# Kernel optimization log

Measured on AMD Instinct MI355X. Metric: run time of the kernel, lower is better.

The kernel has to match this reference:

```python
import jax, jax.numpy as jnp
import numpy as np

V = 25; NE = 5; DIM = 192; H = 6; HD = 32; N = 64; T = 64
SCALE = HD ** -0.5
COEFF = 0.4
NTU_EDGES = [(1,2),(2,21),(3,21),(4,3),(5,21),(6,5),(7,6),(8,7),(9,21),(10,9),(11,10),(12,11),(13,1),(14,13),(15,14),(16,15),(17,1),(18,17),(19,18),(20,19),(22,23),(23,8),(24,25),(25,12)]

def _compute_hops():
    # replicate MHSA.__init__ hop-distance computation (A = [I, adj, adj] summed+binarized)
    adj = np.zeros((V, V))
    for i, j in NTU_EDGES:
        adj[i-1, j-1] = 1.0; adj[j-1, i-1] = 1.0
    h1 = ((np.eye(V) + adj) != 0).astype(np.float64)
    h = [None] * V
    h[0] = np.eye(V); h[1] = h1
    hops = np.zeros((V, V))
    for i in range(2, V):
        h[i] = ((h[i-1] @ h1.T) != 0).astype(np.float64)
    for i in range(V-1, 0, -1):
        if np.any(h[i] - h[i-1]):
            h[i] = h[i] - h[i-1]
            hops += i * h[i]
    return hops.astype(np.int32)

def setup_inputs() -> dict:
    key = jax.random.key(0)
    ks = jax.random.split(key, 12)
    hops = jnp.asarray(_compute_hops())
    n_hop = int(hops.max()) + 1
    std = 0.02
    return {
        "x": jax.random.normal(ks[0], (N, DIM, T, V), jnp.float32),
        "joint_label": jnp.arange(V, dtype=jnp.int32) % NE,  # all 5 hyperedge labels present
        "groups": NE,  # unused by forward (kept for signature fidelity)
        "he_weight": jax.random.uniform(ks[1], (NE,), jnp.float32),
        "hops": hops,
        "ln_g": jnp.ones((DIM,), jnp.float32),
        "ln_b": jnp.zeros((DIM,), jnp.float32),
        "hgc_w": std * jax.random.normal(ks[2], (DIM, DIM), jnp.float32),
        "q_w": std * jax.random.normal(ks[3], (DIM, DIM), jnp.float32),
        "kv_w": std * jax.random.normal(ks[4], (2 * DIM, DIM), jnp.float32),
        "proj_w": std * jax.random.normal(ks[5], (DIM, HD), jnp.float32),  # grouped 1x1 conv, groups=6
        "proj_b": jnp.zeros((DIM,), jnp.float32),
        "rpe": std * jax.random.normal(ks[6], (n_hop, DIM), jnp.float32),
        "w1": std * jax.random.normal(ks[7], (H, HD), jnp.float32),
        "outer": jnp.tile(jnp.eye(V, dtype=jnp.float32), (H, 1, 1)) + std * jax.random.normal(ks[8], (H, V, V), jnp.float32),
        "alpha": 0.1 * jnp.ones((1,), jnp.float32),
        "lin1_w": std * jax.random.normal(ks[9], (T // 5, T), jnp.float32),
        "lin1_b": jnp.zeros((T // 5,), jnp.float32),
        "lin2_w": std * jax.random.normal(ks[10], (T, T // 5), jnp.float32),
        "lin2_b": jnp.zeros((T,), jnp.float32),
    }

def _forward(x, joint_label, he_weight, hops, ln_g, ln_b, hgc_w, q_w, kv_w, proj_w, proj_b, rpe, w1, outer, alpha, lin1_w, lin1_b, lin2_w, lin2_b):
    N_, C, T_, V_ = x.shape
    # ---- HGattn branch: hypergraph conv + temporal squeeze-excite gate ----
    label = jax.nn.one_hot(joint_label, NE, dtype=x.dtype)            # (V, 5)
    label1 = label / label.sum(0, keepdims=True)
    label1 = label1 / jnp.sqrt(label.sum(1, keepdims=True))
    label1 = (he_weight[None, :] * label1).T                          # (5, V)
    norm_label = label / label.sum(1, keepdims=True)
    h_adj = norm_label @ label1                                       # (V, V)
    z = jnp.einsum('nctv,vw->nctw', x, h_adj)
    op = jnp.einsum('nctv,oc->notv', z, hgc_w)                        # (N, dim, T, V) 1x1 conv
    op_tr = op.transpose(0, 1, 3, 2)                                  # (N, dim, V, T)
    s = op_tr.mean(axis=(1, 2))                                       # (N, T) global avg pool over (dim, V)
    g = jax.nn.sigmoid(jax.nn.relu(s @ lin1_w.T + lin1_b) @ lin2_w.T + lin2_b)  # (N, T)
    op_final = op_tr + COEFF * (op_tr * g[:, None, None, :])
    e = op_final.transpose(0, 1, 3, 2)                                # (N, dim, T, V)
    # ---- LayerNorm over channel dim ----
    xc = x.transpose(0, 2, 3, 1)                                      # (N, T, V, C)
    mu = xc.mean(-1, keepdims=True)
    var = xc.var(-1, keepdims=True)
    xn = (((xc - mu) / jnp.sqrt(var + 1e-5)) * ln_g + ln_b).transpose(0, 3, 1, 2)
    # ---- MHSA with hop-indexed relative bias, e-branch scores, outer fusion ----
    q = jnp.einsum('nctv,oc->notv', xn, q_w).reshape(N_, H, HD, T_, V_).transpose(0, 3, 1, 4, 2)   # (N,T,H,V,hd)
    kv = jnp.einsum('nctv,oc->notv', xn, kv_w).reshape(N_, 2, H, HD, T_, V_)
    k = kv[:, 0].transpose(0, 3, 1, 4, 2)
    v = kv[:, 1].transpose(0, 3, 1, 4, 2)
    e_k = e.reshape(N_, H, HD, T_, V_).transpose(0, 3, 1, 4, 2)
    k_r = rpe[hops].reshape(V_, V_, H, HD)                            # hop-distance relative position table
    b = jnp.einsum('bthnc,nmhc->bthnm', q, k_r)
    c = jnp.einsum('bthnc,bthmc->bthnm', q, e_k)
    d = jnp.einsum('hc,bthmc->bthm', w1, e_k)[..., None, :]
    a = jnp.einsum('bthnc,bthmc->bthnm', q, k)
    attn = jax.nn.softmax((a + b + c + d) * SCALE, axis=-1)
    o = jnp.einsum('bthnm,bthmc->bthnc', alpha * attn + outer[None, None], v)
    o = o.transpose(0, 1, 2, 4, 3).reshape(N_, T_, DIM, V_).transpose(0, 2, 1, 3)  # (N, dim, T, V)
    # grouped 1x1 conv projection (groups = H)
    og = o.reshape(N_, H, HD, T_, V_)
    wg = proj_w.reshape(H, HD, HD)
    o = jnp.einsum('ngitv,goi->ngotv', og, wg).reshape(N_, DIM, T_, V_) + proj_b[None, :, None, None]
    return x + o  # dim_in == dim -> identity skip

def reference(x, joint_label, groups, he_weight, hops, ln_g, ln_b, hgc_w, q_w, kv_w, proj_w, proj_b, rpe, w1, outer, alpha, lin1_w, lin1_b, lin2_w, lin2_b):
    return _forward(x, joint_label, he_weight, hops, ln_g, ln_b, hgc_w, q_w, kv_w, proj_w, proj_b, rpe, w1, outer, alpha, lin1_w, lin1_b, lin2_w, lin2_b)
```

## Files before the change

kernel.cpp:

```cpp
#include <hip/hip_runtime.h>
#include <hip/hip_bf16.h>

using bf16 = __hip_bfloat16;
typedef __bf16 bf16x8 __attribute__((ext_vector_type(8)));
typedef float f32x4 __attribute__((ext_vector_type(4)));

constexpr int kDim = 192;
constexpr int kH = 6;
constexpr int kHd = 32;
constexpr int kN = 64;
constexpr int kT = 64;
constexpr int kV = 25;
constexpr int kP = kT * kV;
constexpr int kNCstride = kDim * kP;
constexpr float kScale = 0.17677669529663687f;
constexpr float kCoeff = 0.4f;

__global__ void __launch_bounds__(256) setup_kernel(
    const int* __restrict__ jl, const float* __restrict__ hew,
    const float* __restrict__ hgc, const float* __restrict__ qw,
    const float* __restrict__ kvw, const float* __restrict__ rpe,
    const float* __restrict__ proj_w, const float* __restrict__ lng,
    const float* __restrict__ lnb, int n_hop, float* __restrict__ hadj,
    bf16* __restrict__ Wb, float* __restrict__ G, float* __restrict__ Bb,
    bf16* __restrict__ RPEb, bf16* __restrict__ pwb, bf16* __restrict__ VT) {
  const int bid = blockIdx.x;
  const int tid = threadIdx.x;
  if (bid < 576) {
    int i = bid * 256 + tid;
    float v;
    if (i < 36864) {
      v = hgc[i];
    } else {
      int local = i - 36864;
      int c = local % kDim;
      v = (local < 36864) ? qw[local] : kvw[local - 36864];
      v *= lng[c];
    }
    Wb[i] = __float2bfloat16(v);
  } else if (bid == 576) {
    __shared__ int lbl[kV];
    __shared__ int cnt[8];
    if (tid < 8) cnt[tid] = 0;
    __syncthreads();
    if (tid < kV) { lbl[tid] = jl[tid]; atomicAdd(&cnt[lbl[tid]], 1); }
    __syncthreads();
    for (int idx = tid; idx < kV * kV; idx += 256) {
      int v = idx / kV, w = idx - v * kV;
      float val = 0.f;
      if (lbl[v] == lbl[w]) val = hew[lbl[v]] / (float)cnt[lbl[v]];
      hadj[idx] = val;
    }
  } else if (bid == 577) {
    for (int i = tid; i < kH * 16 * kHd; i += 256) {
      int h = i >> 9, hp = (i >> 5) & 15, d = i & 31;
      float v = (hp < n_hop) ? rpe[hp * kDim + h * kHd + d] : 0.f;
      RPEb[i] = __float2bfloat16(v);
    }
    for (int i = tid; i < kDim * kHd; i += 256)
      pwb[i] = __float2bfloat16(proj_w[i]);
  } else if (bid < 722) {
    int o = (bid - 578) * 4 + (tid >> 6);
    int lane = tid & 63;
    const float* Wr =
        (o < kDim) ? (qw + (size_t)o * kDim) : (kvw + (size_t)(o - kDim) * kDim);
    float gs = 0.f, bs = 0.f;
    for (int c = lane; c < kDim; c += 64) {
      float wv = Wr[c];
      gs += wv * lng[c];
      bs += wv * lnb[c];
    }
    for (int off = 32; off > 0; off >>= 1) {
      gs += __shfl_down(gs, off);
      bs += __shfl_down(bs, off);
    }
    if (lane == 0) { G[o] = gs; Bb[o] = bs; }
  } else {
    int row = (bid - 722) * 256 + tid;
    if (row < kN * kT * kDim) {
      uint4 z = {0u, 0u, 0u, 0u};
      *reinterpret_cast<uint4*>(reinterpret_cast<char*>(VT) + (size_t)row * 64 +
                                48) = z;
    }
  }
}

__global__ void __launch_bounds__(256) prep_kernel(
    const float* __restrict__ x, bf16* __restrict__ XR, float* __restrict__ mu,
    float* __restrict__ rstd) {
  __shared__ float ps[kV][25], ps2[kV][25];
  const int tid = threadIdx.x;
  const int t = blockIdx.x, n = blockIdx.y;
  const float* xb = x + (size_t)n * kNCstride + t * kV;
  size_t ob = ((size_t)n * kP + t * kV) * kDim;
  for (int idx = tid; idx < 600; idx += 256) {
    int p = idx % 25, c8 = idx / 25;
    float a = 0.f, b = 0.f;
    union { uint4 u; __bf16 h[8]; } pk;
#pragma unroll
    for (int i = 0; i < 8; ++i) {
      float v = xb[(size_t)(c8 * 8 + i) * kP + p];
      a += v;
      b += v * v;
      pk.h[i] = (__bf16)v;
    }
    *reinterpret_cast<uint4*>(XR + ob + (size_t)p * kDim + c8 * 8) = pk.u;
    ps[p][c8] = a;
    ps2[p][c8] = b;
  }
  __syncthreads();
  if (tid < kV) {
    float a = 0.f, b = 0.f;
#pragma unroll
    for (int c8 = 0; c8 < 24; ++c8) { a += ps[tid][c8]; b += ps2[tid][c8]; }
    float m = a * (1.f / kDim);
    float var = b * (1.f / kDim) - m * m;
    int gid = n * kP + t * kV + tid;
    mu[gid] = m;
    rstd[gid] = rsqrtf(var + 1e-5f);
  }
}

template <int OBN, int MOUT, bool VS, bool LNF>
__global__ void __launch_bounds__(64) mfma_gemm_kernel(
    const bf16* __restrict__ A, const bf16* __restrict__ B,
    bf16* __restrict__ out, bf16* __restrict__ VT,
    const float* __restrict__ muA, const float* __restrict__ rsA,
    const float* __restrict__ G, const float* __restrict__ Bb) {
  int id = blockIdx.x;
  int per = gridDim.x >> 3;
  int wg = (id & 7) * per + (id >> 3);
  int n = wg / (25 * OBN);
  int rem = wg - n * (25 * OBN);
  const int pb = (rem / OBN) * 64;
  const int ob = (rem % OBN) * 64;
  const int l = threadIdx.x;
  B += (size_t)n * kNCstride;
  out += (size_t)n * kP * MOUT;
  f32x4 acc[4][4] = {};
  const int lm = l & 15;
  const int lk = (l >> 4) * 8;
  for (int kb = 0; kb < kDim; kb += 32) {
    bf16x8 af[4], bfv[4];
#pragma unroll
    for (int mf = 0; mf < 4; ++mf)
      af[mf] = *reinterpret_cast<const bf16x8*>(
          A + (size_t)(ob + mf * 16 + lm) * kDim + kb + lk);
#pragma unroll
    for (int nf = 0; nf < 4; ++nf)
      bfv[nf] = *reinterpret_cast<const bf16x8*>(
          B + (size_t)(pb + nf * 16 + lm) * kDim + kb + lk);
#pragma unroll
    for (int mf = 0; mf < 4; ++mf)
#pragma unroll
      for (int nf = 0; nf < 4; ++nf)
        acc[mf][nf] = __builtin_amdgcn_mfma_f32_16x16x32_bf16(
            af[mf], bfv[nf], acc[mf][nf], 0, 0, 0);
  }
  const int r0 = (l >> 4) * 4;
  float rsv[4], muv[4];
  if (LNF) {
#pragma unroll
    for (int nf = 0; nf < 4; ++nf) {
      int p = pb + nf * 16 + lm;
      rsv[nf] = rsA[n * kP + p];
      muv[nf] = muA[n * kP + p];
    }
  }
  int tt[4], vv[4];
#pragma unroll
  for (int nf = 0; nf < 4; ++nf) {
    int p = pb + nf * 16 + lm;
    tt[nf] = p / 25;
    vv[nf] = p - tt[nf] * 25;
  }
#pragma unroll
  for (int mf = 0; mf < 4; ++mf) {
    const int o0 = ob + mf * 16 + r0;
    float ga[4] = {0.f, 0.f, 0.f, 0.f}, ba[4] = {0.f, 0.f, 0.f, 0.f};
    if (LNF) {
      float4 g4 = *reinterpret_cast<const float4*>(G + o0);
      float4 b4 = *reinterpret_cast<const float4*>(Bb + o0);
      ga[0] = g4.x; ga[1] = g4.y; ga[2] = g4.z; ga[3] = g4.w;
      ba[0] = b4.x; ba[1] = b4.y; ba[2] = b4.z; ba[3] = b4.w;
    }
    if (!VS || o0 < 384) {
#pragma unroll
      for (int nf = 0; nf < 4; ++nf) {
        const int p = pb + nf * 16 + lm;
        union { uint2 u; bf16 b[4]; } pk;
#pragma unroll
        for (int r = 0; r < 4; ++r) {
          float vvv = acc[mf][nf][r];
          if (LNF) vvv = rsv[nf] * (vvv - muv[nf] * ga[r]) + ba[r];
          pk.b[r] = __float2bfloat16(vvv);
        }
        *reinterpret_cast<uint2*>(out + (size_t)p * MOUT + o0) = pk.u;
      }
    } else {
#pragma unroll
      for (int nf = 0; nf < 4; ++nf) {
        size_t rowb =
            ((size_t)(n * kT + tt[nf]) * kDim + (o0 - 384)) * 32 + vv[nf];
#pragma unroll
        for (int r = 0; r < 4; ++r) {
          float vvv = acc[mf][nf][r];
          if (LNF) vvv = rsv[nf] * (vvv - muv[nf] * ga[r]) + ba[r];
          VT[rowb + (size_t)r * 32] = __float2bfloat16(vvv);
        }
      }
    }
  }
}

__global__ void __launch_bounds__(256) haapply_kernel(
    bf16* __restrict__ OP, const float* __restrict__ hadjg,
    float* __restrict__ s_out) {
  __shared__ ushort tile[kV * kDim];
  __shared__ float ha[640];
  __shared__ float red[4];
  const int tid = threadIdx.x;
  const int t = blockIdx.x, n = blockIdx.y;
  size_t base = ((size_t)n * kP + t * kV) * kDim;
  for (int i = tid; i < kV * kV; i += 256) ha[i] = hadjg[i];
  const uint2* src = reinterpret_cast<const uint2*>(OP + base);
  uint2* dst2 = reinterpret_cast<uint2*>(tile);
  for (int i = tid; i < kV * kDim / 4; i += 256) dst2[i] = src[i];
  __syncthreads();
  float ssum = 0.f;
  for (int idx = tid; idx < 600; idx += 256) {
    int c8 = idx % 24, w = idx / 24;
    float acc[8] = {0.f, 0.f, 0.f, 0.f, 0.f, 0.f, 0.f, 0.f};
    for (int v = 0; v < kV; ++v) {
      float coef = ha[v * kV + w];
      union { uint4 u; __bf16 h[8]; } ld;
      ld.u = *reinterpret_cast<const uint4*>(tile + v * kDim + c8 * 8);
#pragma unroll
      for (int j = 0; j < 8; ++j) acc[j] += coef * (float)ld.h[j];
    }
    union { uint4 u; __bf16 h[8]; } pk;
    float s8 = 0.f;
#pragma unroll
    for (int j = 0; j < 8; ++j) { pk.h[j] = (__bf16)acc[j]; s8 += acc[j]; }
    *reinterpret_cast<uint4*>(OP + base + (size_t)w * kDim + c8 * 8) = pk.u;
    ssum += s8;
  }
  for (int off = 32; off > 0; off >>= 1) ssum += __shfl_down(ssum, off);
  if ((tid & 63) == 0) red[tid >> 6] = ssum;
  __syncthreads();
  if (tid == 0)
    s_out[n * kT + t] = (red[0] + red[1] + red[2] + red[3]) *
                        (1.f / (float)(kDim * kV));
}

__global__ void gate_kernel(const float* __restrict__ s,
                            const float* __restrict__ w1l,
                            const float* __restrict__ b1,
                            const float* __restrict__ w2l,
                            const float* __restrict__ b2,
                            float* __restrict__ gatef) {
  __shared__ float sh[kT];
  __shared__ float hid[12];
  int n = blockIdx.x, t = threadIdx.x;
  sh[t] = s[n * kT + t];
  __syncthreads();
  if (t < 12) {
    float a = b1[t];
    for (int j = 0; j < kT; ++j) a += sh[j] * w1l[t * kT + j];
    hid[t] = fmaxf(a, 0.f);
  }
  __syncthreads();
  float a = b2[t];
  for (int j = 0; j < 12; ++j) a += hid[j] * w2l[t * 12 + j];
  float g = 1.f / (1.f + __expf(-a));
  gatef[n * kT + t] = 1.f + kCoeff * g;
}

__global__ void __launch_bounds__(384) attn_kernel(
    const bf16* __restrict__ QK, const bf16* __restrict__ VT,
    const bf16* __restrict__ OP, const float* __restrict__ gatef,
    const int* __restrict__ hops, const bf16* __restrict__ RPEb,
    const float* __restrict__ w1, const float* __restrict__ outer,
    const float* __restrict__ alpha_p, const bf16* __restrict__ pwb,
    const float* __restrict__ proj_b, const float* __restrict__ x,
    float* __restrict__ out) {
  __shared__ ushort wls[kH][2560];
  __shared__ int hopsS[kV][32];
  const int tid = threadIdx.x;
  const int lane = tid & 63;
  const int h = tid >> 6;
  const int t = blockIdx.x, n = blockIdx.y;
  const int nt = n * kT + t;
  const int lm = lane & 15, g = lane >> 4;

  for (int i = tid; i < kV * 32; i += 384) {
    int v = i >> 5, w = i & 31;
    hopsS[v][w] = (w < kV) ? hops[v * kV + w] : 0;
  }
  __syncthreads();

  bf16* Pp = (bf16*)&wls[h][0];
  bf16* OLp = (bf16*)&wls[h][1280];
  float* QRp = (float*)&wls[h][1280];

  const float f = gatef[nt];
  const float alpha = alpha_p[0];
  const bf16* Qbase = QK + (size_t)(n * kP + t * kV) * 384;
  const bf16* Ebase = OP + (size_t)(n * kP + t * kV) * kDim;
  const int colO = h * kHd + g * 8;

  bf16x8 qf[2], kf[2], ef[2];
#pragma unroll
  for (int mf = 0; mf < 2; ++mf) {
    const bf16* row = Qbase + (size_t)(mf * 16 + lm) * 384;
    qf[mf] = *reinterpret_cast<const bf16x8*>(row + colO);
    kf[mf] = *reinterpret_cast<const bf16x8*>(row + kDim + colO);
    ef[mf] = *reinterpret_cast<const bf16x8*>(
        Ebase + (size_t)(mf * 16 + lm) * kDim + colO);
  }
  bf16x8 rf = *reinterpret_cast<const bf16x8*>(RPEb + (h * 16 + lm) * kHd + g * 8);

  float w1v[8];
  {
    float4 wa = *reinterpret_cast<const float4*>(w1 + h * kHd + g * 8);
    float4 wb = *reinterpret_cast<const float4*>(w1 + h * kHd + g * 8 + 4);
    w1v[0] = wa.x; w1v[1] = wa.y; w1v[2] = wa.z; w1v[3] = wa.w;
    w1v[4] = wb.x; w1v[5] = wb.y; w1v[6] = wb.z; w1v[7] = wb.w;
  }
  float dt[2];
#pragma unroll
  for (int nf = 0; nf < 2; ++nf) {
    float a = 0.f;
#pragma unroll
    for (int j = 0; j < 8; ++j) a += w1v[j] * (float)ef[nf][j];
    a += __shfl_xor(a, 16);
    a += __shfl_xor(a, 32);
    dt[nf] = f * a;
  }

  bf16x8 kef[2];
#pragma unroll
  for (int nf = 0; nf < 2; ++nf)
#pragma unroll
    for (int j = 0; j < 8; ++j)
      kef[nf][j] = (__bf16)((float)kf[nf][j] + f * (float)ef[nf][j]);

  f32x4 aK[2][2] = {};
  f32x4 aR[2] = {};
#pragma unroll
  for (int mf = 0; mf < 2; ++mf) {
#pragma unroll
    for (int nf = 0; nf < 2; ++nf)
      aK[mf][nf] =
          __builtin_amdgcn_mfma_f32_16x16x32_bf16(qf[mf], kef[nf], aK[mf][nf], 0, 0, 0);
    aR[mf] = __builtin_amdgcn_mfma_f32_16x16x32_bf16(qf[mf], rf, aR[mf], 0, 0, 0);
  }

#pragma unroll
  for (int mf = 0; mf < 2; ++mf)
#pragma unroll
    for (int r = 0; r < 4; ++r)
      QRp[(mf * 16 + g * 4 + r) * 18 + lm] = aR[mf][r];

  const bool w1ok = (lm + 16) < kV;
#pragma unroll
  for (int mf = 0; mf < 2; ++mf) {
#pragma unroll
    for (int r = 0; r < 4; ++r) {
      int v = mf * 16 + g * 4 + r;
      int vc = v < kV ? v : kV - 1;
      int hp0 = hopsS[vc][lm];
      int hp1 = hopsS[vc][lm + 16];
      float s0 = (aK[mf][0][r] + QRp[v * 18 + hp0] + dt[0]) * kScale;
      float s1 = (aK[mf][1][r] + QRp[v * 18 + hp1] + dt[1]) * kScale;
      if (!w1ok) s1 = -3.0e38f;
      float m = fmaxf(s0, s1);
#pragma unroll
      for (int d = 1; d < 16; d <<= 1) m = fmaxf(m, __shfl_xor(m, d));
      float e0 = __expf(s0 - m);
      float e1 = w1ok ? __expf(s1 - m) : 0.f;
      float sum = e0 + e1;
#pragma unroll
      for (int d = 1; d < 16; d <<= 1) sum += __shfl_xor(sum, d);
      float inv = alpha / sum;
      float o0 = outer[h * (kV * kV) + vc * kV + lm];
      float o1 = w1ok ? outer[h * (kV * kV) + vc * kV + lm + 16] : 0.f;
      Pp[v * 40 + lm] = __float2bfloat16(e0 * inv + o0);
      Pp[v * 40 + lm + 16] = __float2bfloat16(w1ok ? e1 * inv + o1 : 0.f);
    }
  }

  bf16x8 pa[2], vb[2];
#pragma unroll
  for (int mf = 0; mf < 2; ++mf)
    pa[mf] = *reinterpret_cast<const bf16x8*>(Pp + (mf * 16 + lm) * 40 + g * 8);
#pragma unroll
  for (int nf = 0; nf < 2; ++nf)
    vb[nf] = *reinterpret_cast<const bf16x8*>(
        VT + ((size_t)(nt * kDim + h * kHd + nf * 16 + lm)) * 32 + g * 8);
  f32x4 aO[2][2] = {};
#pragma unroll
  for (int mf = 0; mf < 2; ++mf)
#pragma unroll
    for (int nf = 0; nf < 2; ++nf)
      aO[mf][nf] =
          __builtin_amdgcn_mfma_f32_16x16x32_bf16(pa[mf], vb[nf], aO[mf][nf], 0, 0, 0);

#pragma unroll
  for (int mf = 0; mf < 2; ++mf)
#pragma unroll
    for (int nf = 0; nf < 2; ++nf)
#pragma unroll
      for (int r = 0; r < 4; ++r)
        OLp[(mf * 16 + g * 4 + r) * 40 + nf * 16 + lm] =
            __float2bfloat16(aO[mf][nf][r]);

  bf16x8 oa[2], pwf[2];
#pragma unroll
  for (int nf = 0; nf < 2; ++nf)
    oa[nf] = *reinterpret_cast<const bf16x8*>(OLp + (nf * 16 + lm) * 40 + g * 8);
#pragma unroll
  for (int mf = 0; mf < 2; ++mf)
    pwf[mf] = *reinterpret_cast<const bf16x8*>(pwb +
        (h * kHd + mf * 16 + lm) * kHd + g * 8);
  f32x4 aF[2][2] = {};
#pragma unroll
  for (int mf = 0; mf < 2; ++mf)
#pragma unroll
    for (int nf = 0; nf < 2; ++nf)
      aF[mf][nf] =
          __builtin_amdgcn_mfma_f32_16x16x32_bf16(pwf[mf], oa[nf], aF[mf][nf], 0, 0, 0);

#pragma unroll
  for (int mf = 0; mf < 2; ++mf) {
#pragma unroll
    for (int r = 0; r < 4; ++r) {
      int oo = mf * 16 + g * 4 + r;
      int c = h * kHd + oo;
      float pbv = proj_b[c];
      size_t gbase = (size_t)n * kNCstride + (size_t)c * kP + t * kV;
#pragma unroll
      for (int nf = 0; nf < 2; ++nf) {
        int v = nf * 16 + lm;
        if (v < kV) out[gbase + v] = x[gbase + v] + aF[mf][nf][r] + pbv;
      }
    }
  }
}

extern "C" void kernel_launch(void* const* d_in, const int* in_sizes, int n_in,
                              void* d_out, int out_size, void* d_ws,
                              size_t ws_size, hipStream_t stream) {
  const float* x = (const float*)d_in[0];
  const int* joint_label = (const int*)d_in[1];
  const float* he_weight = (const float*)d_in[3];
  const int* hops = (const int*)d_in[4];
  const float* ln_g = (const float*)d_in[5];
  const float* ln_b = (const float*)d_in[6];
  const float* hgc_w = (const float*)d_in[7];
  const float* q_w = (const float*)d_in[8];
  const float* kv_w = (const float*)d_in[9];
  const float* proj_w = (const float*)d_in[10];
  const float* proj_b = (const float*)d_in[11];
  const float* rpe = (const float*)d_in[12];
  const float* w1 = (const float*)d_in[13];
  const float* outer = (const float*)d_in[14];
  const float* alpha = (const float*)d_in[15];
  const float* lin1_w = (const float*)d_in[16];
  const float* lin1_b = (const float*)d_in[17];
  const float* lin2_w = (const float*)d_in[18];
  const float* lin2_b = (const float*)d_in[19];
  const int n_hop = in_sizes[12] / kDim;

  char* w = (char*)d_ws;
  bf16* QK = (bf16*)w;
  w += (size_t)kN * kP * 2 * kDim * 2;
  bf16* XR = (bf16*)w;
  w += (size_t)kN * kP * kDim * 2;
  bf16* OP = (bf16*)w;
  w += (size_t)kN * kP * kDim * 2;
  w += 65536;
  bf16* VT = (bf16*)w;
  w += (size_t)kN * kT * kDim * 32 * 2;
  bf16* Wb = (bf16*)w;
  w += (size_t)768 * kDim * 2;
  bf16* RPEb = (bf16*)w;
  w += (size_t)kH * 16 * kHd * 2;
  bf16* pwb = (bf16*)w;
  w += (size_t)kDim * kHd * 2;
  float* hadj = (float*)w;
  w += 1024 * 4;
  float* s_ws = (float*)w;
  w += kN * kT * 4;
  float* gatef = (float*)w;
  w += kN * kT * 4;
  float* mu = (float*)w;
  w += (size_t)kN * kP * 4;
  float* rstd = (float*)w;
  w += (size_t)kN * kP * 4;
  float* G = (float*)w;
  w += 576 * 4;
  float* Bb = (float*)w;
  w += 576 * 4;

  hipLaunchKernelGGL(setup_kernel, dim3(3794), dim3(256), 0, stream,
                     joint_label, he_weight, hgc_w, q_w, kv_w, rpe, proj_w,
                     ln_g, ln_b, n_hop, hadj, Wb, G, Bb, RPEb, pwb, VT);
  hipLaunchKernelGGL(prep_kernel, dim3(kT, kN), dim3(256), 0, stream, x, XR,
                     mu, rstd);
  hipLaunchKernelGGL((mfma_gemm_kernel<3, kDim, false, false>),
                     dim3(25 * 3 * kN), dim3(64), 0, stream, Wb, XR, OP,
                     (bf16*)nullptr, nullptr, nullptr, nullptr, nullptr);
  hipLaunchKernelGGL(haapply_kernel, dim3(kT, kN), dim3(256), 0, stream, OP,
                     hadj, s_ws);
  hipLaunchKernelGGL(gate_kernel, dim3(kN), dim3(kT), 0, stream, s_ws, lin1_w,
                     lin1_b, lin2_w, lin2_b, gatef);
  hipLaunchKernelGGL((mfma_gemm_kernel<9, 384, true, true>),
                     dim3(25 * 9 * kN), dim3(64), 0, stream, Wb + 192 * kDim,
                     XR, QK, VT, mu, rstd, G, Bb);
  hipLaunchKernelGGL(attn_kernel, dim3(kT, kN), dim3(384), 0, stream, QK, VT,
                     OP, gatef, hops, RPEb, w1, outer, alpha, pwb, proj_b, x,
                     (float*)d_out);
}
```

Measured before the change: 354.6 us.

## Fuse QKV projection GEMM into attention kernel, drop QK/VT buffers

Removes the separate QKV GEMM launch and its QK and transposed VT intermediate buffers. Each attention wave now computes its head's Q, K and V projections from XR directly with MFMA, applies the LayerNorm fold in registers, and stages the results in shared memory. The relative-position scores are read with cross-lane shuffles instead of a shared-memory table, and the hops table is stored as bytes. The setup kernel no longer zero-pads VT. This trades global write and read traffic for extra weight loads and longer per-block work in the attention kernel.

```diff
diff --git a/kernel.cpp b/kernel.cpp
--- a/kernel.cpp
+++ b/kernel.cpp
@@ -23,7 +23,7 @@
     const float* __restrict__ proj_w, const float* __restrict__ lng,
     const float* __restrict__ lnb, int n_hop, float* __restrict__ hadj,
     bf16* __restrict__ Wb, float* __restrict__ G, float* __restrict__ Bb,
-    bf16* __restrict__ RPEb, bf16* __restrict__ pwb, bf16* __restrict__ VT) {
+    bf16* __restrict__ RPEb, bf16* __restrict__ pwb) {
   const int bid = blockIdx.x;
   const int tid = threadIdx.x;
   if (bid < 576) {
@@ -59,7 +59,7 @@
     }
     for (int i = tid; i < kDim * kHd; i += 256)
       pwb[i] = __float2bfloat16(proj_w[i]);
-  } else if (bid < 722) {
+  } else {
     int o = (bid - 578) * 4 + (tid >> 6);
     int lane = tid & 63;
     const float* Wr =
@@ -75,13 +75,6 @@
       bs += __shfl_down(bs, off);
     }
     if (lane == 0) { G[o] = gs; Bb[o] = bs; }
-  } else {
-    int row = (bid - 722) * 256 + tid;
-    if (row < kN * kT * kDim) {
-      uint4 z = {0u, 0u, 0u, 0u};
-      *reinterpret_cast<uint4*>(reinterpret_cast<char*>(VT) + (size_t)row * 64 +
-                                48) = z;
-    }
   }
 }
 
@@ -121,22 +114,19 @@
   }
 }
 
-template <int OBN, int MOUT, bool VS, bool LNF>
 __global__ void __launch_bounds__(64) mfma_gemm_kernel(
     const bf16* __restrict__ A, const bf16* __restrict__ B,
-    bf16* __restrict__ out, bf16* __restrict__ VT,
-    const float* __restrict__ muA, const float* __restrict__ rsA,
-    const float* __restrict__ G, const float* __restrict__ Bb) {
+    bf16* __restrict__ out) {
   int id = blockIdx.x;
   int per = gridDim.x >> 3;
   int wg = (id & 7) * per + (id >> 3);
-  int n = wg / (25 * OBN);
-  int rem = wg - n * (25 * OBN);
-  const int pb = (rem / OBN) * 64;
-  const int ob = (rem % OBN) * 64;
+  int n = wg / (25 * 3);
+  int rem = wg - n * (25 * 3);
+  const int pb = (rem / 3) * 64;
+  const int ob = (rem % 3) * 64;
   const int l = threadIdx.x;
   B += (size_t)n * kNCstride;
-  out += (size_t)n * kP * MOUT;
+  out += (size_t)n * kP * kDim;
   f32x4 acc[4][4] = {};
   const int lm = l & 15;
   const int lk = (l >> 4) * 8;
@@ -158,57 +148,16 @@
             af[mf], bfv[nf], acc[mf][nf], 0, 0, 0);
   }
   const int r0 = (l >> 4) * 4;
-  float rsv[4], muv[4];
-  if (LNF) {
-#pragma unroll
-    for (int nf = 0; nf < 4; ++nf) {
-      int p = pb + nf * 16 + lm;
-      rsv[nf] = rsA[n * kP + p];
-      muv[nf] = muA[n * kP + p];
-    }
-  }
-  int tt[4], vv[4];
-#pragma unroll
-  for (int nf = 0; nf < 4; ++nf) {
-    int p = pb + nf * 16 + lm;
-    tt[nf] = p / 25;
-    vv[nf] = p - tt[nf] * 25;
-  }
 #pragma unroll
   for (int mf = 0; mf < 4; ++mf) {
     const int o0 = ob + mf * 16 + r0;
-    float ga[4] = {0.f, 0.f, 0.f, 0.f}, ba[4] = {0.f, 0.f, 0.f, 0.f};
-    if (LNF) {
-      float4 g4 = *reinterpret_cast<const float4*>(G + o0);
-      float4 b4 = *reinterpret_cast<const float4*>(Bb + o0);
-      ga[0] = g4.x; ga[1] = g4.y; ga[2] = g4.z; ga[3] = g4.w;
-      ba[0] = b4.x; ba[1] = b4.y; ba[2] = b4.z; ba[3] = b4.w;
-    }
-    if (!VS || o0 < 384) {
-#pragma unroll
-      for (int nf = 0; nf < 4; ++nf) {
-        const int p = pb + nf * 16 + lm;
-        union { uint2 u; bf16 b[4]; } pk;
-#pragma unroll
-        for (int r = 0; r < 4; ++r) {
-          float vvv = acc[mf][nf][r];
-          if (LNF) vvv = rsv[nf] * (vvv - muv[nf] * ga[r]) + ba[r];
-          pk.b[r] = __float2bfloat16(vvv);
-        }
-        *reinterpret_cast<uint2*>(out + (size_t)p * MOUT + o0) = pk.u;
-      }
-    } else {
-#pragma unroll
-      for (int nf = 0; nf < 4; ++nf) {
-        size_t rowb =
-            ((size_t)(n * kT + tt[nf]) * kDim + (o0 - 384)) * 32 + vv[nf];
-#pragma unroll
-        for (int r = 0; r < 4; ++r) {
-          float vvv = acc[mf][nf][r];
-          if (LNF) vvv = rsv[nf] * (vvv - muv[nf] * ga[r]) + ba[r];
-          VT[rowb + (size_t)r * 32] = __float2bfloat16(vvv);
-        }
-      }
+#pragma unroll
+    for (int nf = 0; nf < 4; ++nf) {
+      const int p = pb + nf * 16 + lm;
+      union { uint2 u; bf16 b[4]; } pk;
+#pragma unroll
+      for (int r = 0; r < 4; ++r) pk.b[r] = __float2bfloat16(acc[mf][nf][r]);
+      *reinterpret_cast<uint2*>(out + (size_t)p * kDim + o0) = pk.u;
     }
   }
 }
@@ -277,7 +226,9 @@
 }
 
 __global__ void __launch_bounds__(384) attn_kernel(
-    const bf16* __restrict__ QK, const bf16* __restrict__ VT,
+    const bf16* __restrict__ XR, const bf16* __restrict__ Wqkv,
+    const float* __restrict__ mu, const float* __restrict__ rstd,
+    const float* __restrict__ G, const float* __restrict__ Bb,
     const bf16* __restrict__ OP, const float* __restrict__ gatef,
     const int* __restrict__ hops, const bf16* __restrict__ RPEb,
     const float* __restrict__ w1, const float* __restrict__ outer,
@@ -285,7 +236,7 @@
     const float* __restrict__ proj_b, const float* __restrict__ x,
     float* __restrict__ out) {
   __shared__ ushort wls[kH][2560];
-  __shared__ int hopsS[kV][32];
+  __shared__ unsigned char hopsB[kV][32];
   const int tid = threadIdx.x;
   const int lane = tid & 63;
   const int h = tid >> 6;
@@ -295,28 +246,84 @@
 
   for (int i = tid; i < kV * 32; i += 384) {
     int v = i >> 5, w = i & 31;
-    hopsS[v][w] = (w < kV) ? hops[v * kV + w] : 0;
+    hopsB[v][w] = (w < kV) ? (unsigned char)hops[v * kV + w] : 0;
   }
   __syncthreads();
 
-  bf16* Pp = (bf16*)&wls[h][0];
-  bf16* OLp = (bf16*)&wls[h][1280];
-  float* QRp = (float*)&wls[h][1280];
+  bf16* buf0 = (bf16*)&wls[h][0];
+  bf16* buf1 = (bf16*)&wls[h][1280];
 
   const float f = gatef[nt];
   const float alpha = alpha_p[0];
-  const bf16* Qbase = QK + (size_t)(n * kP + t * kV) * 384;
-  const bf16* Ebase = OP + (size_t)(n * kP + t * kV) * kDim;
-  const int colO = h * kHd + g * 8;
+  const bf16* XRb = XR + ((size_t)n * kP + (size_t)t * kV) * kDim;
+  const bf16* Ebase = OP + ((size_t)n * kP + (size_t)t * kV) * kDim;
+
+  float rsv[2], muv[2];
+#pragma unroll
+  for (int nf = 0; nf < 2; ++nf) {
+    int p = n * kP + t * kV + nf * 16 + lm;
+    int pc = min(p, kN * kP - 1);
+    rsv[nf] = rstd[pc];
+    muv[nf] = mu[pc];
+  }
+
+  const bf16* WQ = Wqkv + (size_t)(h * kHd) * kDim;
+  const bf16* WK = Wqkv + (size_t)(kDim + h * kHd) * kDim;
+  f32x4 aQ[2][2] = {}, aKg[2][2] = {};
+#pragma unroll
+  for (int kb = 0; kb < kDim; kb += 32) {
+    bf16x8 xf[2], wq[2], wk[2];
+#pragma unroll
+    for (int nf = 0; nf < 2; ++nf)
+      xf[nf] = *reinterpret_cast<const bf16x8*>(
+          XRb + (size_t)(nf * 16 + lm) * kDim + kb + g * 8);
+#pragma unroll
+    for (int jf = 0; jf < 2; ++jf) {
+      wq[jf] = *reinterpret_cast<const bf16x8*>(
+          WQ + (size_t)(jf * 16 + lm) * kDim + kb + g * 8);
+      wk[jf] = *reinterpret_cast<const bf16x8*>(
+          WK + (size_t)(jf * 16 + lm) * kDim + kb + g * 8);
+    }
+#pragma unroll
+    for (int jf = 0; jf < 2; ++jf)
+#pragma unroll
+      for (int nf = 0; nf < 2; ++nf) {
+        aQ[jf][nf] = __builtin_amdgcn_mfma_f32_16x16x32_bf16(wq[jf], xf[nf],
+                                                             aQ[jf][nf], 0, 0, 0);
+        aKg[jf][nf] = __builtin_amdgcn_mfma_f32_16x16x32_bf16(wk[jf], xf[nf],
+                                                              aKg[jf][nf], 0, 0, 0);
+      }
+  }
+#pragma unroll
+  for (int jf = 0; jf < 2; ++jf) {
+    int o0 = h * kHd + jf * 16 + g * 4;
+    float4 gq = *reinterpret_cast<const float4*>(G + o0);
+    float4 bq = *reinterpret_cast<const float4*>(Bb + o0);
+    float4 gk = *reinterpret_cast<const float4*>(G + kDim + o0);
+    float4 bk = *reinterpret_cast<const float4*>(Bb + kDim + o0);
+    float gqa[4] = {gq.x, gq.y, gq.z, gq.w}, bqa[4] = {bq.x, bq.y, bq.z, bq.w};
+    float gka[4] = {gk.x, gk.y, gk.z, gk.w}, bka[4] = {bk.x, bk.y, bk.z, bk.w};
+#pragma unroll
+    for (int nf = 0; nf < 2; ++nf) {
+      int row = (nf * 16 + lm) * 40 + jf * 16 + g * 4;
+#pragma unroll
+      for (int r = 0; r < 4; ++r) {
+        buf0[row + r] = __float2bfloat16(
+            rsv[nf] * (aQ[jf][nf][r] - muv[nf] * gqa[r]) + bqa[r]);
+        buf1[row + r] = __float2bfloat16(
+            rsv[nf] * (aKg[jf][nf][r] - muv[nf] * gka[r]) + bka[r]);
+      }
+    }
+  }
+  asm volatile("" ::: "memory");
 
   bf16x8 qf[2], kf[2], ef[2];
 #pragma unroll
   for (int mf = 0; mf < 2; ++mf) {
-    const bf16* row = Qbase + (size_t)(mf * 16 + lm) * 384;
-    qf[mf] = *reinterpret_cast<const bf16x8*>(row + colO);
-    kf[mf] = *reinterpret_cast<const bf16x8*>(row + kDim + colO);
+    qf[mf] = *reinterpret_cast<const bf16x8*>(buf0 + (mf * 16 + lm) * 40 + g * 8);
+    kf[mf] = *reinterpret_cast<const bf16x8*>(buf1 + (mf * 16 + lm) * 40 + g * 8);
     ef[mf] = *reinterpret_cast<const bf16x8*>(
-        Ebase + (size_t)(mf * 16 + lm) * kDim + colO);
+        Ebase + (size_t)(mf * 16 + lm) * kDim + h * kHd + g * 8);
   }
   bf16x8 rf = *reinterpret_cast<const bf16x8*>(RPEb + (h * 16 + lm) * kHd + g * 8);
 
@@ -337,7 +344,6 @@
     a += __shfl_xor(a, 32);
     dt[nf] = f * a;
   }
-
   bf16x8 kef[2];
 #pragma unroll
   for (int nf = 0; nf < 2; ++nf)
@@ -345,34 +351,31 @@
     for (int j = 0; j < 8; ++j)
       kef[nf][j] = (__bf16)((float)kf[nf][j] + f * (float)ef[nf][j]);
 
-  f32x4 aK[2][2] = {};
+  f32x4 aS[2][2] = {};
   f32x4 aR[2] = {};
 #pragma unroll
   for (int mf = 0; mf < 2; ++mf) {
 #pragma unroll
     for (int nf = 0; nf < 2; ++nf)
-      aK[mf][nf] =
-          __builtin_amdgcn_mfma_f32_16x16x32_bf16(qf[mf], kef[nf], aK[mf][nf], 0, 0, 0);
+      aS[mf][nf] = __builtin_amdgcn_mfma_f32_16x16x32_bf16(qf[mf], kef[nf],
+                                                           aS[mf][nf], 0, 0, 0);
     aR[mf] = __builtin_amdgcn_mfma_f32_16x16x32_bf16(qf[mf], rf, aR[mf], 0, 0, 0);
   }
 
-#pragma unroll
-  for (int mf = 0; mf < 2; ++mf)
-#pragma unroll
-    for (int r = 0; r < 4; ++r)
-      QRp[(mf * 16 + g * 4 + r) * 18 + lm] = aR[mf][r];
-
   const bool w1ok = (lm + 16) < kV;
+  bf16* Pp = buf0;
 #pragma unroll
   for (int mf = 0; mf < 2; ++mf) {
 #pragma unroll
     for (int r = 0; r < 4; ++r) {
       int v = mf * 16 + g * 4 + r;
       int vc = v < kV ? v : kV - 1;
-      int hp0 = hopsS[vc][lm];
-      int hp1 = hopsS[vc][lm + 16];
-      float s0 = (aK[mf][0][r] + QRp[v * 18 + hp0] + dt[0]) * kScale;
-      float s1 = (aK[mf][1][r] + QRp[v * 18 + hp1] + dt[1]) * kScale;
+      int hp0 = hopsB[vc][lm];
+      int hp1 = hopsB[vc][lm + 16];
+      float qr0 = __shfl(aR[mf][r], g * 16 + hp0);
+      float qr1 = __shfl(aR[mf][r], g * 16 + hp1);
+      float s0 = (aS[mf][0][r] + qr0 + dt[0]) * kScale;
+      float s1 = (aS[mf][1][r] + qr1 + dt[1]) * kScale;
       if (!w1ok) s1 = -3.0e38f;
       float m = fmaxf(s0, s1);
 #pragma unroll
@@ -389,6 +392,44 @@
       Pp[v * 40 + lm + 16] = __float2bfloat16(w1ok ? e1 * inv + o1 : 0.f);
     }
   }
+  asm volatile("" ::: "memory");
+
+  const bf16* WV = Wqkv + (size_t)(2 * kDim + h * kHd) * kDim;
+  f32x4 aV[2][2] = {};
+#pragma unroll
+  for (int kb = 0; kb < kDim; kb += 32) {
+    bf16x8 xf[2], wv[2];
+#pragma unroll
+    for (int nf = 0; nf < 2; ++nf)
+      xf[nf] = *reinterpret_cast<const bf16x8*>(
+          XRb + (size_t)(nf * 16 + lm) * kDim + kb + g * 8);
+#pragma unroll
+    for (int jf = 0; jf < 2; ++jf)
+      wv[jf] = *reinterpret_cast<const bf16x8*>(
+          WV + (size_t)(jf * 16 + lm) * kDim + kb + g * 8);
+#pragma unroll
+    for (int jf = 0; jf < 2; ++jf)
+#pragma unroll
+      for (int nf = 0; nf < 2; ++nf)
+        aV[jf][nf] = __builtin_amdgcn_mfma_f32_16x16x32_bf16(wv[jf], xf[nf],
+                                                             aV[jf][nf], 0, 0, 0);
+  }
+  bf16* VTp = buf1;
+#pragma unroll
+  for (int jf = 0; jf < 2; ++jf) {
+    int o0 = 2 * kDim + h * kHd + jf * 16 + g * 4;
+    float4 gv = *reinterpret_cast<const float4*>(G + o0);
+    float4 bv = *reinterpret_cast<const float4*>(Bb + o0);
+    float gva[4] = {gv.x, gv.y, gv.z, gv.w}, bva[4] = {bv.x, bv.y, bv.z, bv.w};
+#pragma unroll
+    for (int nf = 0; nf < 2; ++nf)
+#pragma unroll
+      for (int r = 0; r < 4; ++r) {
+        float val = rsv[nf] * (aV[jf][nf][r] - muv[nf] * gva[r]) + bva[r];
+        VTp[(jf * 16 + g * 4 + r) * 40 + nf * 16 + lm] = __float2bfloat16(val);
+      }
+  }
+  asm volatile("" ::: "memory");
 
   bf16x8 pa[2], vb[2];
 #pragma unroll
@@ -396,8 +437,7 @@
     pa[mf] = *reinterpret_cast<const bf16x8*>(Pp + (mf * 16 + lm) * 40 + g * 8);
 #pragma unroll
   for (int nf = 0; nf < 2; ++nf)
-    vb[nf] = *reinterpret_cast<const bf16x8*>(
-        VT + ((size_t)(nt * kDim + h * kHd + nf * 16 + lm)) * 32 + g * 8);
+    vb[nf] = *reinterpret_cast<const bf16x8*>(VTp + (nf * 16 + lm) * 40 + g * 8);
   f32x4 aO[2][2] = {};
 #pragma unroll
   for (int mf = 0; mf < 2; ++mf)
@@ -405,7 +445,9 @@
     for (int nf = 0; nf < 2; ++nf)
       aO[mf][nf] =
           __builtin_amdgcn_mfma_f32_16x16x32_bf16(pa[mf], vb[nf], aO[mf][nf], 0, 0, 0);
-
+  asm volatile("" ::: "memory");
+
+  bf16* OLp = buf0;
 #pragma unroll
   for (int mf = 0; mf < 2; ++mf)
 #pragma unroll
@@ -473,15 +515,11 @@
   const int n_hop = in_sizes[12] / kDim;
 
   char* w = (char*)d_ws;
-  bf16* QK = (bf16*)w;
-  w += (size_t)kN * kP * 2 * kDim * 2;
   bf16* XR = (bf16*)w;
   w += (size_t)kN * kP * kDim * 2;
   bf16* OP = (bf16*)w;
   w += (size_t)kN * kP * kDim * 2;
   w += 65536;
-  bf16* VT = (bf16*)w;
-  w += (size_t)kN * kT * kDim * 32 * 2;
   bf16* Wb = (bf16*)w;
   w += (size_t)768 * kDim * 2;
   bf16* RPEb = (bf16*)w;
@@ -503,22 +541,18 @@
   float* Bb = (float*)w;
   w += 576 * 4;
 
-  hipLaunchKernelGGL(setup_kernel, dim3(3794), dim3(256), 0, stream,
+  hipLaunchKernelGGL(setup_kernel, dim3(722), dim3(256), 0, stream,
                      joint_label, he_weight, hgc_w, q_w, kv_w, rpe, proj_w,
-                     ln_g, ln_b, n_hop, hadj, Wb, G, Bb, RPEb, pwb, VT);
+                     ln_g, ln_b, n_hop, hadj, Wb, G, Bb, RPEb, pwb);
   hipLaunchKernelGGL(prep_kernel, dim3(kT, kN), dim3(256), 0, stream, x, XR,
                      mu, rstd);
-  hipLaunchKernelGGL((mfma_gemm_kernel<3, kDim, false, false>),
-                     dim3(25 * 3 * kN), dim3(64), 0, stream, Wb, XR, OP,
-                     (bf16*)nullptr, nullptr, nullptr, nullptr, nullptr);
+  hipLaunchKernelGGL(mfma_gemm_kernel, dim3(25 * 3 * kN), dim3(64), 0, stream,
+                     Wb, XR, OP);
   hipLaunchKernelGGL(haapply_kernel, dim3(kT, kN), dim3(256), 0, stream, OP,
                      hadj, s_ws);
   hipLaunchKernelGGL(gate_kernel, dim3(kN), dim3(kT), 0, stream, s_ws, lin1_w,
                      lin1_b, lin2_w, lin2_b, gatef);
-  hipLaunchKernelGGL((mfma_gemm_kernel<9, 384, true, true>),
-                     dim3(25 * 9 * kN), dim3(64), 0, stream, Wb + 192 * kDim,
-                     XR, QK, VT, mu, rstd, G, Bb);
-  hipLaunchKernelGGL(attn_kernel, dim3(kT, kN), dim3(384), 0, stream, QK, VT,
-                     OP, gatef, hops, RPEb, w1, outer, alpha, pwb, proj_b, x,
-                     (float*)d_out);
-}
+  hipLaunchKernelGGL(attn_kernel, dim3(kT, kN), dim3(384), 0, stream, XR,
+                     Wb + (size_t)192 * kDim, mu, rstd, G, Bb, OP, gatef, hops,
+                     RPEb, w1, outer, alpha, pwb, proj_b, x, (float*)d_out);
+}
```

Result: slower. 378.3 us (+6.7%).

## Add dedicated QKV GEMM with LDS-staged V transpose and trim attention LDS

Applied to the files above, without the earlier changes.

Splits the QKV projection into its own kernel. It tiles over 50-position blocks, so each tile covers exactly two time steps, and stages the V output through shared memory. From there it writes coalesced, zero-padded VT rows, which replaces the scattered 2-byte stores and removes the separate VT zero-fill pass in setup. The attention kernel looks up the relative-position scores with lane shuffles instead of an LDS round trip, stores hops as bytes, and shrinks its LDS footprint. It also hoists the VT, proj-weight and outer loads ahead of the barrier so their latency overlaps with compute. The 50-wide tiles leave part of each 64-wide MFMA tile unused, which adds redundant compute.

```diff
diff --git a/kernel.cpp b/kernel.cpp
--- a/kernel.cpp
+++ b/kernel.cpp
@@ -23,7 +23,7 @@
     const float* __restrict__ proj_w, const float* __restrict__ lng,
     const float* __restrict__ lnb, int n_hop, float* __restrict__ hadj,
     bf16* __restrict__ Wb, float* __restrict__ G, float* __restrict__ Bb,
-    bf16* __restrict__ RPEb, bf16* __restrict__ pwb, bf16* __restrict__ VT) {
+    bf16* __restrict__ RPEb, bf16* __restrict__ pwb) {
   const int bid = blockIdx.x;
   const int tid = threadIdx.x;
   if (bid < 576) {
@@ -59,7 +59,7 @@
     }
     for (int i = tid; i < kDim * kHd; i += 256)
       pwb[i] = __float2bfloat16(proj_w[i]);
-  } else if (bid < 722) {
+  } else {
     int o = (bid - 578) * 4 + (tid >> 6);
     int lane = tid & 63;
     const float* Wr =
@@ -75,13 +75,6 @@
       bs += __shfl_down(bs, off);
     }
     if (lane == 0) { G[o] = gs; Bb[o] = bs; }
-  } else {
-    int row = (bid - 722) * 256 + tid;
-    if (row < kN * kT * kDim) {
-      uint4 z = {0u, 0u, 0u, 0u};
-      *reinterpret_cast<uint4*>(reinterpret_cast<char*>(VT) + (size_t)row * 64 +
-                                48) = z;
-    }
   }
 }
 
@@ -121,22 +114,19 @@
   }
 }
 
-template <int OBN, int MOUT, bool VS, bool LNF>
 __global__ void __launch_bounds__(64) mfma_gemm_kernel(
     const bf16* __restrict__ A, const bf16* __restrict__ B,
-    bf16* __restrict__ out, bf16* __restrict__ VT,
-    const float* __restrict__ muA, const float* __restrict__ rsA,
-    const float* __restrict__ G, const float* __restrict__ Bb) {
+    bf16* __restrict__ out) {
   int id = blockIdx.x;
   int per = gridDim.x >> 3;
   int wg = (id & 7) * per + (id >> 3);
-  int n = wg / (25 * OBN);
-  int rem = wg - n * (25 * OBN);
-  const int pb = (rem / OBN) * 64;
-  const int ob = (rem % OBN) * 64;
+  int n = wg / (25 * 3);
+  int rem = wg - n * (25 * 3);
+  const int pb = (rem / 3) * 64;
+  const int ob = (rem % 3) * 64;
   const int l = threadIdx.x;
   B += (size_t)n * kNCstride;
-  out += (size_t)n * kP * MOUT;
+  out += (size_t)n * kP * kDim;
   f32x4 acc[4][4] = {};
   const int lm = l & 15;
   const int lk = (l >> 4) * 8;
@@ -158,57 +148,121 @@
             af[mf], bfv[nf], acc[mf][nf], 0, 0, 0);
   }
   const int r0 = (l >> 4) * 4;
-  float rsv[4], muv[4];
-  if (LNF) {
-#pragma unroll
-    for (int nf = 0; nf < 4; ++nf) {
-      int p = pb + nf * 16 + lm;
-      rsv[nf] = rsA[n * kP + p];
-      muv[nf] = muA[n * kP + p];
-    }
-  }
-  int tt[4], vv[4];
-#pragma unroll
-  for (int nf = 0; nf < 4; ++nf) {
-    int p = pb + nf * 16 + lm;
-    tt[nf] = p / 25;
-    vv[nf] = p - tt[nf] * 25;
-  }
 #pragma unroll
   for (int mf = 0; mf < 4; ++mf) {
     const int o0 = ob + mf * 16 + r0;
-    float ga[4] = {0.f, 0.f, 0.f, 0.f}, ba[4] = {0.f, 0.f, 0.f, 0.f};
-    if (LNF) {
+#pragma unroll
+    for (int nf = 0; nf < 4; ++nf) {
+      const int p = pb + nf * 16 + lm;
+      union { uint2 u; bf16 b[4]; } pk;
+#pragma unroll
+      for (int r = 0; r < 4; ++r) pk.b[r] = __float2bfloat16(acc[mf][nf][r]);
+      *reinterpret_cast<uint2*>(out + (size_t)p * kDim + o0) = pk.u;
+    }
+  }
+}
+
+__global__ void __launch_bounds__(64) gemm_qkv_kernel(
+    const bf16* __restrict__ A, const bf16* __restrict__ B,
+    bf16* __restrict__ QK, bf16* __restrict__ VT,
+    const float* __restrict__ muA, const float* __restrict__ rsA,
+    const float* __restrict__ G, const float* __restrict__ Bb) {
+  __shared__ ushort vt_s[64 * 52];
+  int id = blockIdx.x;
+  int per = gridDim.x >> 3;
+  int wg = (id & 7) * per + (id >> 3);
+  int n = wg / 288;
+  int rem = wg - n * 288;
+  const int pt = rem / 9;
+  const int ob = rem % 9;
+  const int pb = pt * 50;
+  const int l = threadIdx.x;
+  B += (size_t)n * kNCstride;
+  f32x4 acc[4][4] = {};
+  const int lm = l & 15;
+  const int lk = (l >> 4) * 8;
+  for (int kb = 0; kb < kDim; kb += 32) {
+    bf16x8 af[4], bfv[4];
+#pragma unroll
+    for (int mf = 0; mf < 4; ++mf)
+      af[mf] = *reinterpret_cast<const bf16x8*>(
+          A + (size_t)(ob * 64 + mf * 16 + lm) * kDim + kb + lk);
+#pragma unroll
+    for (int nf = 0; nf < 4; ++nf)
+      bfv[nf] = *reinterpret_cast<const bf16x8*>(
+          B + (size_t)(pb + nf * 16 + lm) * kDim + kb + lk);
+#pragma unroll
+    for (int mf = 0; mf < 4; ++mf)
+#pragma unroll
+      for (int nf = 0; nf < 4; ++nf)
+        acc[mf][nf] = __builtin_amdgcn_mfma_f32_16x16x32_bf16(
+            af[mf], bfv[nf], acc[mf][nf], 0, 0, 0);
+  }
+  const int r0 = (l >> 4) * 4;
+  float rsv[4], muv[4];
+#pragma unroll
+  for (int nf = 0; nf < 4; ++nf) {
+    int pidx = n * kP + min(pb + nf * 16 + lm, kP - 1);
+    rsv[nf] = rsA[pidx];
+    muv[nf] = muA[pidx];
+  }
+  if (ob < 6) {
+    QK += (size_t)n * kP * 384;
+#pragma unroll
+    for (int mf = 0; mf < 4; ++mf) {
+      const int o0 = ob * 64 + mf * 16 + r0;
       float4 g4 = *reinterpret_cast<const float4*>(G + o0);
       float4 b4 = *reinterpret_cast<const float4*>(Bb + o0);
-      ga[0] = g4.x; ga[1] = g4.y; ga[2] = g4.z; ga[3] = g4.w;
-      ba[0] = b4.x; ba[1] = b4.y; ba[2] = b4.z; ba[3] = b4.w;
-    }
-    if (!VS || o0 < 384) {
+      float ga[4] = {g4.x, g4.y, g4.z, g4.w};
+      float ba[4] = {b4.x, b4.y, b4.z, b4.w};
 #pragma unroll
       for (int nf = 0; nf < 4; ++nf) {
-        const int p = pb + nf * 16 + lm;
-        union { uint2 u; bf16 b[4]; } pk;
-#pragma unroll
-        for (int r = 0; r < 4; ++r) {
-          float vvv = acc[mf][nf][r];
-          if (LNF) vvv = rsv[nf] * (vvv - muv[nf] * ga[r]) + ba[r];
-          pk.b[r] = __float2bfloat16(vvv);
-        }
-        *reinterpret_cast<uint2*>(out + (size_t)p * MOUT + o0) = pk.u;
-      }
-    } else {
-#pragma unroll
-      for (int nf = 0; nf < 4; ++nf) {
-        size_t rowb =
-            ((size_t)(n * kT + tt[nf]) * kDim + (o0 - 384)) * 32 + vv[nf];
-#pragma unroll
-        for (int r = 0; r < 4; ++r) {
-          float vvv = acc[mf][nf][r];
-          if (LNF) vvv = rsv[nf] * (vvv - muv[nf] * ga[r]) + ba[r];
-          VT[rowb + (size_t)r * 32] = __float2bfloat16(vvv);
+        int pl = nf * 16 + lm;
+        if (pl < 50) {
+          union { uint2 u; bf16 b[4]; } pk;
+#pragma unroll
+          for (int r = 0; r < 4; ++r)
+            pk.b[r] = __float2bfloat16(
+                rsv[nf] * (acc[mf][nf][r] - muv[nf] * ga[r]) + ba[r]);
+          *reinterpret_cast<uint2*>(QK + (size_t)(pb + pl) * 384 + o0) = pk.u;
         }
       }
+    }
+  } else {
+    const int d0 = (ob - 6) * 64;
+    bf16* vt_b = reinterpret_cast<bf16*>(vt_s);
+#pragma unroll
+    for (int mf = 0; mf < 4; ++mf) {
+      const int o0 = 384 + d0 + mf * 16 + r0;
+      float4 g4 = *reinterpret_cast<const float4*>(G + o0);
+      float4 b4 = *reinterpret_cast<const float4*>(Bb + o0);
+      float ga[4] = {g4.x, g4.y, g4.z, g4.w};
+      float ba[4] = {b4.x, b4.y, b4.z, b4.w};
+#pragma unroll
+      for (int nf = 0; nf < 4; ++nf) {
+        int pl = nf * 16 + lm;
+        if (pl < 50) {
+#pragma unroll
+          for (int r = 0; r < 4; ++r)
+            vt_b[(mf * 16 + r0 + r) * 52 + pl] = __float2bfloat16(
+                rsv[nf] * (acc[mf][nf][r] - muv[nf] * ga[r]) + ba[r]);
+        }
+      }
+    }
+#pragma unroll
+    for (int it = 0; it < 16; ++it) {
+      int rowi = it * 8 + (l >> 3);
+      int tsel = rowi >> 6, olocal = rowi & 63;
+      int vcol = (l & 7) * 4;
+      union { uint2 u; ushort s[4]; } pk;
+#pragma unroll
+      for (int q = 0; q < 4; ++q) {
+        int v = vcol + q;
+        pk.s[q] = (v < kV) ? vt_s[olocal * 52 + tsel * 25 + v] : (ushort)0;
+      }
+      size_t addr =
+          ((size_t)(n * kT + pt * 2 + tsel) * kDim + d0 + olocal) * 32 + vcol;
+      *reinterpret_cast<uint2*>(VT + addr) = pk.u;
     }
   }
 }
@@ -284,31 +338,19 @@
     const float* __restrict__ alpha_p, const bf16* __restrict__ pwb,
     const float* __restrict__ proj_b, const float* __restrict__ x,
     float* __restrict__ out) {
-  __shared__ ushort wls[kH][2560];
-  __shared__ int hopsS[kV][32];
+  __shared__ ushort wls[kH][1280];
+  __shared__ unsigned char hopsB[kV][32];
   const int tid = threadIdx.x;
   const int lane = tid & 63;
   const int h = tid >> 6;
   const int t = blockIdx.x, n = blockIdx.y;
   const int nt = n * kT + t;
   const int lm = lane & 15, g = lane >> 4;
-
-  for (int i = tid; i < kV * 32; i += 384) {
-    int v = i >> 5, w = i & 31;
-    hopsS[v][w] = (w < kV) ? hops[v * kV + w] : 0;
-  }
-  __syncthreads();
-
-  bf16* Pp = (bf16*)&wls[h][0];
-  bf16* OLp = (bf16*)&wls[h][1280];
-  float* QRp = (float*)&wls[h][1280];
-
-  const float f = gatef[nt];
-  const float alpha = alpha_p[0];
-  const bf16* Qbase = QK + (size_t)(n * kP + t * kV) * 384;
-  const bf16* Ebase = OP + (size_t)(n * kP + t * kV) * kDim;
+  const bool w1ok = (lm + 16) < kV;
+
+  const bf16* Qbase = QK + (size_t)(nt * kV) * 384;
+  const bf16* Ebase = OP + (size_t)(nt * kV) * kDim;
   const int colO = h * kHd + g * 8;
-
   bf16x8 qf[2], kf[2], ef[2];
 #pragma unroll
   for (int mf = 0; mf < 2; ++mf) {
@@ -319,7 +361,14 @@
         Ebase + (size_t)(mf * 16 + lm) * kDim + colO);
   }
   bf16x8 rf = *reinterpret_cast<const bf16x8*>(RPEb + (h * 16 + lm) * kHd + g * 8);
-
+  bf16x8 vb[2], pwf[2];
+#pragma unroll
+  for (int nf = 0; nf < 2; ++nf) {
+    vb[nf] = *reinterpret_cast<const bf16x8*>(
+        VT + ((size_t)(nt * kDim + h * kHd + nf * 16 + lm)) * 32 + g * 8);
+    pwf[nf] = *reinterpret_cast<const bf16x8*>(
+        pwb + (h * kHd + nf * 16 + lm) * kHd + g * 8);
+  }
   float w1v[8];
   {
     float4 wa = *reinterpret_cast<const float4*>(w1 + h * kHd + g * 8);
@@ -327,6 +376,27 @@
     w1v[0] = wa.x; w1v[1] = wa.y; w1v[2] = wa.z; w1v[3] = wa.w;
     w1v[4] = wb.x; w1v[5] = wb.y; w1v[6] = wb.z; w1v[7] = wb.w;
   }
+  float outv0[8], outv1[8];
+#pragma unroll
+  for (int mf = 0; mf < 2; ++mf)
+#pragma unroll
+    for (int r = 0; r < 4; ++r) {
+      int v = mf * 16 + g * 4 + r;
+      int vc = v < kV ? v : kV - 1;
+      const float* orow = outer + h * (kV * kV) + vc * kV;
+      outv0[mf * 4 + r] = orow[lm];
+      outv1[mf * 4 + r] = w1ok ? orow[lm + 16] : 0.f;
+    }
+  const float f = gatef[nt];
+  const float alpha = alpha_p[0];
+
+  for (int i = tid; i < kV * 32; i += 384) {
+    int v = i >> 5, w = i & 31;
+    hopsB[v][w] = (w < kV) ? (unsigned char)hops[v * kV + w] : 0;
+  }
+  __syncthreads();
+  bf16* Pp = (bf16*)&wls[h][0];
+
   float dt[2];
 #pragma unroll
   for (int nf = 0; nf < 2; ++nf) {
@@ -337,7 +407,6 @@
     a += __shfl_xor(a, 32);
     dt[nf] = f * a;
   }
-
   bf16x8 kef[2];
 #pragma unroll
   for (int nf = 0; nf < 2; ++nf)
@@ -345,34 +414,29 @@
     for (int j = 0; j < 8; ++j)
       kef[nf][j] = (__bf16)((float)kf[nf][j] + f * (float)ef[nf][j]);
 
-  f32x4 aK[2][2] = {};
+  f32x4 aS[2][2] = {};
   f32x4 aR[2] = {};
 #pragma unroll
   for (int mf = 0; mf < 2; ++mf) {
 #pragma unroll
     for (int nf = 0; nf < 2; ++nf)
-      aK[mf][nf] =
-          __builtin_amdgcn_mfma_f32_16x16x32_bf16(qf[mf], kef[nf], aK[mf][nf], 0, 0, 0);
+      aS[mf][nf] = __builtin_amdgcn_mfma_f32_16x16x32_bf16(qf[mf], kef[nf],
+                                                           aS[mf][nf], 0, 0, 0);
     aR[mf] = __builtin_amdgcn_mfma_f32_16x16x32_bf16(qf[mf], rf, aR[mf], 0, 0, 0);
   }
 
-#pragma unroll
-  for (int mf = 0; mf < 2; ++mf)
-#pragma unroll
-    for (int r = 0; r < 4; ++r)
-      QRp[(mf * 16 + g * 4 + r) * 18 + lm] = aR[mf][r];
-
-  const bool w1ok = (lm + 16) < kV;
 #pragma unroll
   for (int mf = 0; mf < 2; ++mf) {
 #pragma unroll
     for (int r = 0; r < 4; ++r) {
       int v = mf * 16 + g * 4 + r;
       int vc = v < kV ? v : kV - 1;
-      int hp0 = hopsS[vc][lm];
-      int hp1 = hopsS[vc][lm + 16];
-      float s0 = (aK[mf][0][r] + QRp[v * 18 + hp0] + dt[0]) * kScale;
-      float s1 = (aK[mf][1][r] + QRp[v * 18 + hp1] + dt[1]) * kScale;
+      int hp0 = hopsB[vc][lm];
+      int hp1 = hopsB[vc][lm + 16];
+      float qr0 = __shfl(aR[mf][r], g * 16 + hp0);
+      float qr1 = __shfl(aR[mf][r], g * 16 + hp1);
+      float s0 = (aS[mf][0][r] + qr0 + dt[0]) * kScale;
+      float s1 = (aS[mf][1][r] + qr1 + dt[1]) * kScale;
       if (!w1ok) s1 = -3.0e38f;
       float m = fmaxf(s0, s1);
 #pragma unroll
@@ -383,21 +447,16 @@
 #pragma unroll
       for (int d = 1; d < 16; d <<= 1) sum += __shfl_xor(sum, d);
       float inv = alpha / sum;
-      float o0 = outer[h * (kV * kV) + vc * kV + lm];
-      float o1 = w1ok ? outer[h * (kV * kV) + vc * kV + lm + 16] : 0.f;
-      Pp[v * 40 + lm] = __float2bfloat16(e0 * inv + o0);
-      Pp[v * 40 + lm + 16] = __float2bfloat16(w1ok ? e1 * inv + o1 : 0.f);
-    }
-  }
-
-  bf16x8 pa[2], vb[2];
+      Pp[v * 40 + lm] = __float2bfloat16(e0 * inv + outv0[mf * 4 + r]);
+      Pp[v * 40 + lm + 16] =
+          __float2bfloat16(w1ok ? e1 * inv + outv1[mf * 4 + r] : 0.f);
+    }
+  }
+
+  bf16x8 pa[2];
 #pragma unroll
   for (int mf = 0; mf < 2; ++mf)
     pa[mf] = *reinterpret_cast<const bf16x8*>(Pp + (mf * 16 + lm) * 40 + g * 8);
-#pragma unroll
-  for (int nf = 0; nf < 2; ++nf)
-    vb[nf] = *reinterpret_cast<const bf16x8*>(
-        VT + ((size_t)(nt * kDim + h * kHd + nf * 16 + lm)) * 32 + g * 8);
   f32x4 aO[2][2] = {};
 #pragma unroll
   for (int mf = 0; mf < 2; ++mf)
@@ -412,17 +471,12 @@
     for (int nf = 0; nf < 2; ++nf)
 #pragma unroll
       for (int r = 0; r < 4; ++r)
-        OLp[(mf * 16 + g * 4 + r) * 40 + nf * 16 + lm] =
+        Pp[(mf * 16 + g * 4 + r) * 40 + nf * 16 + lm] =
             __float2bfloat16(aO[mf][nf][r]);
-
-  bf16x8 oa[2], pwf[2];
+  bf16x8 oa[2];
 #pragma unroll
   for (int nf = 0; nf < 2; ++nf)
-    oa[nf] = *reinterpret_cast<const bf16x8*>(OLp + (nf * 16 + lm) * 40 + g * 8);
-#pragma unroll
-  for (int mf = 0; mf < 2; ++mf)
-    pwf[mf] = *reinterpret_cast<const bf16x8*>(pwb +
-        (h * kHd + mf * 16 + lm) * kHd + g * 8);
+    oa[nf] = *reinterpret_cast<const bf16x8*>(Pp + (nf * 16 + lm) * 40 + g * 8);
   f32x4 aF[2][2] = {};
 #pragma unroll
   for (int mf = 0; mf < 2; ++mf)
@@ -503,21 +557,19 @@
   float* Bb = (float*)w;
   w += 576 * 4;
 
-  hipLaunchKernelGGL(setup_kernel, dim3(3794), dim3(256), 0, stream,
+  hipLaunchKernelGGL(setup_kernel, dim3(722), dim3(256), 0, stream,
                      joint_label, he_weight, hgc_w, q_w, kv_w, rpe, proj_w,
-                     ln_g, ln_b, n_hop, hadj, Wb, G, Bb, RPEb, pwb, VT);
+                     ln_g, ln_b, n_hop, hadj, Wb, G, Bb, RPEb, pwb);
   hipLaunchKernelGGL(prep_kernel, dim3(kT, kN), dim3(256), 0, stream, x, XR,
                      mu, rstd);
-  hipLaunchKernelGGL((mfma_gemm_kernel<3, kDim, false, false>),
-                     dim3(25 * 3 * kN), dim3(64), 0, stream, Wb, XR, OP,
-                     (bf16*)nullptr, nullptr, nullptr, nullptr, nullptr);
+  hipLaunchKernelGGL(mfma_gemm_kernel, dim3(25 * 3 * kN), dim3(64), 0, stream,
+                     Wb, XR, OP);
   hipLaunchKernelGGL(haapply_kernel, dim3(kT, kN), dim3(256), 0, stream, OP,
                      hadj, s_ws);
   hipLaunchKernelGGL(gate_kernel, dim3(kN), dim3(kT), 0, stream, s_ws, lin1_w,
                      lin1_b, lin2_w, lin2_b, gatef);
-  hipLaunchKernelGGL((mfma_gemm_kernel<9, 384, true, true>),
-                     dim3(25 * 9 * kN), dim3(64), 0, stream, Wb + 192 * kDim,
-                     XR, QK, VT, mu, rstd, G, Bb);
+  hipLaunchKernelGGL(gemm_qkv_kernel, dim3(32 * 9 * kN), dim3(64), 0, stream,
+                     Wb + (size_t)192 * kDim, XR, QK, VT, mu, rstd, G, Bb);
   hipLaunchKernelGGL(attn_kernel, dim3(kT, kN), dim3(384), 0, stream, QK, VT,
                      OP, gatef, hops, RPEb, w1, outer, alpha, pwb, proj_b, x,
                      (float*)d_out);
```

New measurement: 374.1 us. 5.5% more time.
